# Optimization experiments

Hardware: AMD Instinct MI355X
Metric: run time of the kernel (lower is better)

## Reference

```python
import jax, jax.numpy as jnp
import numpy as np

IN_DIM = 256
OUT_DIM = 256
EMBED_DIM = 256
GROUPS = 8
BN_EPS = 1e-5


def conv2d(x, w, b, pad, groups=1):
    # x: NCHW, w: OIHW (I = in_ch / groups)
    out = jax.lax.conv_general_dilated(
        x, w, window_strides=(1, 1), padding=[(pad, pad), (pad, pad)],
        dimension_numbers=('NCHW', 'OIHW', 'NCHW'), feature_group_count=groups)
    return out + b[None, :, None, None]


def setup_inputs() -> dict:
    key = jax.random.key(0)
    ks = jax.random.split(key, 8)
    s = 0.05
    d = {}
    d['x'] = jax.random.normal(ks[0], (2, IN_DIM, 16, 16), jnp.float32)
    d['y'] = jax.random.normal(ks[1], (2, OUT_DIM, 128, 128), jnp.float32)
    # channle_reduce: Conv2d(256, 64, k=3, groups=64) -> weight (64, 4, 3, 3)
    d['w_cr'] = jax.random.normal(ks[2], (IN_DIM // 4, 4, 3, 3), jnp.float32) * s
    d['b_cr'] = jnp.zeros((IN_DIM // 4,), jnp.float32)
    # depthwise convs on 64 channels
    d['w_dw3'] = jax.random.normal(ks[3], (IN_DIM // 4, 1, 3, 3), jnp.float32) * s
    d['b_dw3'] = jnp.zeros((IN_DIM // 4,), jnp.float32)
    d['w_dw7'] = jax.random.normal(ks[4], (IN_DIM // 4, 1, 5, 5), jnp.float32) * s
    d['b_dw7'] = jnp.zeros((IN_DIM // 4,), jnp.float32)
    # gate: Conv2d(256, 128, 1) + BN + StarReLU
    d['w_gate'] = jax.random.normal(ks[5], (IN_DIM // 2, IN_DIM, 1, 1), jnp.float32) * s
    d['b_gate'] = jnp.zeros((IN_DIM // 2,), jnp.float32)
    d['bn_gamma'] = jnp.ones((IN_DIM // 2,), jnp.float32)
    d['bn_beta'] = jnp.zeros((IN_DIM // 2,), jnp.float32)
    d['bn_mean'] = jnp.zeros((IN_DIM // 2,), jnp.float32)
    d['bn_var'] = jnp.ones((IN_DIM // 2,), jnp.float32)
    d['sr_scale'] = jnp.ones((1,), jnp.float32)
    d['sr_bias'] = jnp.zeros((1,), jnp.float32)
    # linear1: Linear(16, 8192) -> torch weight shape (8192, 16)
    d['w_lin'] = jax.random.normal(ks[6], (OUT_DIM * EMBED_DIM // GROUPS, IN_DIM // (2 * GROUPS)), jnp.float32) * s
    d['b_lin'] = jnp.zeros((OUT_DIM * EMBED_DIM // GROUPS,), jnp.float32)
    return d


def reference(x, y, w_cr, b_cr, w_dw3, b_dw3, w_dw7, b_dw7, w_gate, b_gate,
              bn_gamma, bn_beta, bn_mean, bn_var, sr_scale, sr_bias, w_lin, b_lin):
    B, C, H, Wd = x.shape
    # gate branch: 1x1 conv -> BN (inference stats) -> StarReLU
    g = conv2d(x, w_gate, b_gate, 0)
    inv = (bn_gamma / jnp.sqrt(bn_var + BN_EPS))[None, :, None, None]
    g = (g - bn_mean[None, :, None, None]) * inv + bn_beta[None, :, None, None]
    g = sr_scale * jnp.square(jnp.maximum(g, 0.0)) + sr_bias
    # feature branch
    xr = conv2d(x, w_cr, b_cr, 1, groups=IN_DIM // 4)        # (B, 64, H, W)
    x3 = conv2d(xr, w_dw3, b_dw3, 1, groups=IN_DIM // 4)
    x7 = conv2d(xr, w_dw7, b_dw7, 2, groups=IN_DIM // 4)
    xc = jnp.concatenate([x3, x7], axis=1) * g               # (B, 128, H, W)
    # per-pixel weight generation: (B,H,W,G,16) @ (16,8192)
    xc = xc.reshape(B, GROUPS, -1, H, Wd).transpose(0, 3, 4, 1, 2)
    wdec = jnp.einsum('bhwgi,oi->bhwgo', xc, w_lin) + b_lin  # (B,H,W,8,8192)
    # flatten (G, out*embed/G) -> (embed, out); matches torch reshape order
    wdec = wdec.reshape(B, H, Wd, EMBED_DIM, OUT_DIM)
    # patch-wise dynamic 1x1 conv == per-patch batched matmul
    b, c, h, w = y.shape
    fh, fw = H, Wd
    ph, pw = h // fh, w // fw
    yp = y.reshape(b, c, fh, ph, fw, pw)
    # out[b,e,f,p,g,q] = sum_c wdec[b,f,g,e,c] * y[b,c,f,p,g,q]
    out = jnp.einsum('bfgec,bcfpgq->befpgq', wdec, yp)
    return out.reshape(b, EMBED_DIM, h, w)
```

## Files before the change

### kernel.cpp

```cpp
#include <hip/hip_runtime.h>
#include <stdint.h>


typedef __attribute__((ext_vector_type(8))) short short8;
typedef __attribute__((ext_vector_type(4))) float f32x4;

#define BN_EPS 1e-5f

__device__ __forceinline__ unsigned short f2bf(float f) {
  unsigned u = __float_as_uint(f);
  return (unsigned short)((u + 0x8000u) >> 16);
}
__device__ __forceinline__ unsigned pk2bf(float a, float b) {
  unsigned ua = __float_as_uint(a), ub = __float_as_uint(b);
  return ((ua + 0x8000u) >> 16) | ((ub + 0x8000u) & 0xFFFF0000u);
}

__global__ __launch_bounds__(256) void k1a_groupconv(
    const float* __restrict__ x, const float* __restrict__ w_cr,
    const float* __restrict__ b_cr, float* __restrict__ xr)
{
  __shared__ float xs[4][256];
  int b = blockIdx.x >> 6, cr = blockIdx.x & 63;
  int t = threadIdx.x;
  {
    int ch = t >> 6, off = (t & 63) * 4;
    float4 v = *(const float4*)(x + b * 65536 + (cr * 4 + ch) * 256 + off);
    *(float4*)&xs[ch][off] = v;
  }
  __syncthreads();
  int h = t >> 4, w = t & 15;
  float a = b_cr[cr];
  #pragma unroll
  for (int ii = 0; ii < 4; ++ii) {
    const float* wp = w_cr + (cr * 4 + ii) * 9;
    #pragma unroll
    for (int ky = 0; ky < 3; ++ky) {
      int gy = h + ky - 1;
      #pragma unroll
      for (int kx = 0; kx < 3; ++kx) {
        int gx = w + kx - 1;
        float v = (gy >= 0 && gy < 16 && gx >= 0 && gx < 16) ? xs[ii][gy * 16 + gx] : 0.f;
        a += wp[ky * 3 + kx] * v;
      }
    }
  }
  xr[(b * 64 + cr) * 256 + t] = a;
}

__global__ __launch_bounds__(256) void k1b_gate_dw(
    const float* __restrict__ x, const float* __restrict__ xr,
    const float* __restrict__ w_dw3, const float* __restrict__ b_dw3,
    const float* __restrict__ w_dw7, const float* __restrict__ b_dw7,
    const float* __restrict__ w_gate, const float* __restrict__ b_gate,
    const float* __restrict__ bn_gamma, const float* __restrict__ bn_beta,
    const float* __restrict__ bn_mean, const float* __restrict__ bn_var,
    const float* __restrict__ sr_scale, const float* __restrict__ sr_bias,
    const float* __restrict__ w_lin, short* __restrict__ wlin_bf, short* __restrict__ xc_bf)
{
  __shared__ float xcen[256];
  __shared__ float gs[128];
  int blk = blockIdx.x;
  int b = blk >> 8, h = (blk >> 4) & 15, w = blk & 15;
  int t = threadIdx.x;

  { int idx = blk * 256 + t; wlin_bf[idx] = (short)f2bf(w_lin[idx]); }

  xcen[t] = x[b * 65536 + t * 256 + h * 16 + w];
  __syncthreads();

  int o = t >> 1, half = t & 1;
  {
    const float* wrow = w_gate + o * 256 + half * 128;
    const float* xcn  = xcen + half * 128;
    float ga = 0.f;
    #pragma unroll 8
    for (int ci = 0; ci < 128; ci += 4) {
      float4 wv = *(const float4*)(wrow + ci);
      float4 xv = *(const float4*)(xcn + ci);
      ga += wv.x * xv.x + wv.y * xv.y + wv.z * xv.z + wv.w * xv.w;
    }
    ga += __shfl_xor(ga, 1);
    float inv = bn_gamma[o] * rsqrtf(bn_var[o] + BN_EPS);
    float gg = (ga + b_gate[o] - bn_mean[o]) * inv + bn_beta[o];
    gg = fmaxf(gg, 0.f);
    gg = sr_scale[0] * gg * gg + sr_bias[0];
    if (half == 0) gs[o] = gg;
  }
  __syncthreads();

  if (t < 128) {
    int oc = t;
    float f0;
    if (oc < 64) {
      f0 = b_dw3[oc];
      const float* wp = w_dw3 + oc * 9;
      const float* xp = xr + (b * 64 + oc) * 256;
      #pragma unroll
      for (int ky = 0; ky < 3; ++ky) {
        int gy = h + ky - 1;
        #pragma unroll
        for (int kx = 0; kx < 3; ++kx) {
          int gx = w + kx - 1;
          float v = (gy >= 0 && gy < 16 && gx >= 0 && gx < 16) ? xp[gy * 16 + gx] : 0.f;
          f0 += wp[ky * 3 + kx] * v;
        }
      }
    } else {
      int c5 = oc - 64;
      f0 = b_dw7[c5];
      const float* wp = w_dw7 + c5 * 25;
      const float* xp = xr + (b * 64 + c5) * 256;
      #pragma unroll
      for (int ky = 0; ky < 5; ++ky) {
        int gy = h + ky - 2;
        #pragma unroll
        for (int kx = 0; kx < 5; ++kx) {
          int gx = w + kx - 2;
          float v = (gy >= 0 && gy < 16 && gx >= 0 && gx < 16) ? xp[gy * 16 + gx] : 0.f;
          f0 += wp[ky * 5 + kx] * v;
        }
      }
    }
    int pix = (b * 16 + h) * 16 + w;
    xc_bf[pix * 128 + oc] = (short)f2bf(f0 * gs[oc]);
  }
}

__global__ __launch_bounds__(256) void k2a_wgen(
    const short* __restrict__ wlin_bf, const short* __restrict__ xc_bf,
    const float* __restrict__ b_lin, short* __restrict__ wd)
{
  __shared__ __align__(16) short Wt[16 * 2048];
  int blk = blockIdx.x;
  int n0 = (blk >> 2) * 16;
  int oc = (blk & 3) * 2048;
  int tid = threadIdx.x;
  int wave = tid >> 6, lane = tid & 63;
  int quad = lane >> 4, l16 = lane & 15;

  short8 af = {0, 0, 0, 0, 0, 0, 0, 0};
  if (quad < 2) af = *(const short8*)(xc_bf + (n0 + l16) * 16 + quad * 8);

  f32x4 zero4 = {0.f, 0.f, 0.f, 0.f};
  #pragma unroll 8
  for (int i = 0; i < 32; ++i) {
    int o0 = wave * 512 + i * 16;
    short8 bf = {0, 0, 0, 0, 0, 0, 0, 0};
    if (quad < 2) bf = *(const short8*)(wlin_bf + (oc + o0 + l16) * 16 + quad * 8);
    f32x4 d = __builtin_amdgcn_mfma_f32_16x16x32_bf16(af, bf, zero4, 0, 0, 0);
    float bl = b_lin[oc + o0 + l16];
    #pragma unroll
    for (int r = 0; r < 4; ++r)
      Wt[(quad * 4 + r) * 2048 + o0 + l16] = (short)f2bf(d[r] + bl);
  }
  __syncthreads();

  const uint2* src = (const uint2*)Wt;
  #pragma unroll 8
  for (int j = 0; j < 32; ++j) {
    int fl = j * 256 + tid;
    int row = fl >> 9;
    int col = (fl & 511) * 4;
    *(uint2*)(wd + (size_t)(n0 + row) * 8192 + oc + col) = src[fl];
  }
}

__global__ __launch_bounds__(512, 6) void k2b_dynconv(
    const float* __restrict__ y, const short* __restrict__ wd,
    float* __restrict__ out)
{
  __shared__ __align__(16) short Ylds[16384];
  __shared__ __align__(16) float scratch[4096];

  int phys = blockIdx.x;
  int blk = (phys & 7) * 64 + (phys >> 3);
  int b = blk >> 8, f = (blk >> 4) & 15, g = blk & 15;
  int tid = threadIdx.x;
  int wave = tid >> 6, lane = tid & 63;
  int quad = lane >> 4, l16 = lane & 15;

  const float* yb = y + b * 4194304 + (f * 8) * 128 + g * 8;
  const short* wdp = wd + (size_t)(((b * 16 + f) * 16 + g)) * 65536;

  int c_a = (tid >> 4) & 63;
  (void)c_a;
  float4 v0, v1, w0, w1;
  {
    int task0 = tid, task1 = 512 + tid;
    int ca = task0 >> 4, pfa = task0 & 15;
    int cb = task1 >> 4, pfb = task1 & 15;
    v0 = *(const float4*)(yb + ca * 16384 + (pfa >> 1) * 128 + (pfa & 1) * 4);
    v1 = *(const float4*)(yb + cb * 16384 + (pfb >> 1) * 128 + (pfb & 1) * 4);
  }
  for (int pass = 0; pass < 4; ++pass) {
    {
      int task0 = tid, task1 = 512 + tid;
      int ca = task0 >> 4, pfa = task0 & 15;
      int cb = task1 >> 4, pfb = task1 & 15;
      *(float4*)&scratch[ca * 64 + pfa * 4] = v0;
      *(float4*)&scratch[cb * 64 + pfb * 4] = v1;
      if (pass < 3) {
        w0 = *(const float4*)(yb + ((pass + 1) * 64 + ca) * 16384 + (pfa >> 1) * 128 + (pfa & 1) * 4);
        w1 = *(const float4*)(yb + ((pass + 1) * 64 + cb) * 16384 + (pfb >> 1) * 128 + (pfb & 1) * 4);
      }
    }
    __syncthreads();
    {
      int pix = tid & 63, cg = tid >> 6;
      float s0 = scratch[(cg * 8 + 0) * 64 + pix];
      float s1 = scratch[(cg * 8 + 1) * 64 + pix];
      float s2 = scratch[(cg * 8 + 2) * 64 + pix];
      float s3 = scratch[(cg * 8 + 3) * 64 + pix];
      float s4 = scratch[(cg * 8 + 4) * 64 + pix];
      float s5 = scratch[(cg * 8 + 5) * 64 + pix];
      float s6 = scratch[(cg * 8 + 6) * 64 + pix];
      float s7 = scratch[(cg * 8 + 7) * 64 + pix];
      uint4 pk;
      pk.x = pk2bf(s0, s1); pk.y = pk2bf(s2, s3);
      pk.z = pk2bf(s4, s5); pk.w = pk2bf(s6, s7);
      int chunk = pass * 8 + cg;
      int physc = chunk ^ (pix & 7);
      *(uint4*)&Ylds[pix * 256 + physc * 8] = pk;
    }
    __syncthreads();
    v0 = w0; v1 = w1;
  }

  f32x4 acc[2][4];
  f32x4 zero4 = {0.f, 0.f, 0.f, 0.f};
  #pragma unroll
  for (int et = 0; et < 2; ++et)
    #pragma unroll
    for (int nt = 0; nt < 4; ++nt)
      acc[et][nt] = zero4;

  #pragma unroll 2
  for (int cc = 0; cc < 8; ++cc) {
    short8 A[2], Bf[4];
    #pragma unroll
    for (int et = 0; et < 2; ++et) {
      int e = wave * 32 + et * 16 + l16;
      A[et] = *(const short8*)(wdp + e * 256 + cc * 32 + quad * 8);
    }
    int chunk = cc * 4 + quad;
    #pragma unroll
    for (int nt = 0; nt < 4; ++nt) {
      int nn = nt * 16 + l16;
      int physc = chunk ^ (nn & 7);
      Bf[nt] = *(const short8*)&Ylds[nn * 256 + physc * 8];
    }
    #pragma unroll
    for (int et = 0; et < 2; ++et)
      #pragma unroll
      for (int nt = 0; nt < 4; ++nt)
        acc[et][nt] = __builtin_amdgcn_mfma_f32_16x16x32_bf16(A[et], Bf[nt], acc[et][nt], 0, 0, 0);
  }

  float* ob = out + b * 4194304 + (f * 8) * 128 + g * 8;
  #pragma unroll
  for (int et = 0; et < 2; ++et) {
    int e0 = wave * 32 + et * 16 + quad * 4;
    #pragma unroll
    for (int nt = 0; nt < 4; ++nt) {
      int pix = nt * 16 + l16;
      float* oa = ob + (pix >> 3) * 128 + (pix & 7);
      #pragma unroll
      for (int r = 0; r < 4; ++r)
        oa[(e0 + r) * 16384] = acc[et][nt][r];
    }
  }
}

extern "C" void kernel_launch(void* const* d_in, const int* in_sizes, int n_in,
                              void* d_out, int out_size, void* d_ws, size_t ws_size,
                              hipStream_t stream) {
  const float* x        = (const float*)d_in[0];
  const float* y        = (const float*)d_in[1];
  const float* w_cr     = (const float*)d_in[2];
  const float* b_cr     = (const float*)d_in[3];
  const float* w_dw3    = (const float*)d_in[4];
  const float* b_dw3    = (const float*)d_in[5];
  const float* w_dw7    = (const float*)d_in[6];
  const float* b_dw7    = (const float*)d_in[7];
  const float* w_gate   = (const float*)d_in[8];
  const float* b_gate   = (const float*)d_in[9];
  const float* bn_gamma = (const float*)d_in[10];
  const float* bn_beta  = (const float*)d_in[11];
  const float* bn_mean  = (const float*)d_in[12];
  const float* bn_var   = (const float*)d_in[13];
  const float* sr_scale = (const float*)d_in[14];
  const float* sr_bias  = (const float*)d_in[15];
  const float* w_lin    = (const float*)d_in[16];
  const float* b_lin    = (const float*)d_in[17];
  float* out = (float*)d_out;

  short* xc_bf   = (short*)d_ws;
  short* wlin_bf = (short*)((char*)d_ws + 131072);
  float* xr      = (float*)((char*)d_ws + 131072 + 262144);
  short* wd      = (short*)((char*)d_ws + 131072 + 262144 + 131072);

  hipLaunchKernelGGL(k1a_groupconv, dim3(128), dim3(256), 0, stream, x, w_cr, b_cr, xr);
  hipLaunchKernelGGL(k1b_gate_dw, dim3(512), dim3(256), 0, stream,
                     x, xr, w_dw3, b_dw3, w_dw7, b_dw7, w_gate, b_gate,
                     bn_gamma, bn_beta, bn_mean, bn_var, sr_scale, sr_bias,
                     w_lin, wlin_bf, xc_bf);
  hipLaunchKernelGGL(k2a_wgen, dim3(1024), dim3(256), 0, stream,
                     wlin_bf, xc_bf, b_lin, wd);
  hipLaunchKernelGGL(k2b_dynconv, dim3(512), dim3(512), 0, stream, y, wd, out);
}
```

Measured before the change: 174.5 us.

## Split dynamic-conv blocks into half-patches to double grid size

The dynamic 1x1 conv kernel now launches 1024 blocks, each handling half of an 8x8 patch (4 rows, 32 pixels) instead of the full patch. Shared Y staging is halved, and the software-prefetch double buffering of y loads is removed in favour of two simple load passes. The aim is more parallelism and occupancy across CUs. The cost is that each per-patch weight matrix (wd) is now read by two blocks, which doubles weight traffic, and there is less MFMA work per loaded A fragment.

Result: slower. 180.6 us (+3.5%).

```diff
diff --git a/kernel.cpp b/kernel.cpp
--- a/kernel.cpp
+++ b/kernel.cpp
@@ -170,74 +170,64 @@
     const float* __restrict__ y, const short* __restrict__ wd,
     float* __restrict__ out)
 {
-  __shared__ __align__(16) short Ylds[16384];
+  __shared__ __align__(16) short Ylds[8192];
   __shared__ __align__(16) float scratch[4096];
 
   int phys = blockIdx.x;
-  int blk = (phys & 7) * 64 + (phys >> 3);
-  int b = blk >> 8, f = (blk >> 4) & 15, g = blk & 15;
+  int x_ = phys & 7, q_ = phys >> 3;
+  int sub = q_ & 3, pphi = q_ >> 2;
+  int pp = pphi * 8 + x_;
+  int b = pp >> 7, f = (pp >> 3) & 15, gp = pp & 7;
+  int g = gp * 2 + (sub & 1);
+  int half = sub >> 1;
+
   int tid = threadIdx.x;
   int wave = tid >> 6, lane = tid & 63;
   int quad = lane >> 4, l16 = lane & 15;
 
-  const float* yb = y + b * 4194304 + (f * 8) * 128 + g * 8;
+  const float* yb = y + b * 4194304 + (f * 8 + half * 4) * 128 + g * 8;
   const short* wdp = wd + (size_t)(((b * 16 + f) * 16 + g)) * 65536;
 
-  int c_a = (tid >> 4) & 63;
-  (void)c_a;
-  float4 v0, v1, w0, w1;
-  {
-    int task0 = tid, task1 = 512 + tid;
-    int ca = task0 >> 4, pfa = task0 & 15;
-    int cb = task1 >> 4, pfb = task1 & 15;
-    v0 = *(const float4*)(yb + ca * 16384 + (pfa >> 1) * 128 + (pfa & 1) * 4);
-    v1 = *(const float4*)(yb + cb * 16384 + (pfb >> 1) * 128 + (pfb & 1) * 4);
-  }
-  for (int pass = 0; pass < 4; ++pass) {
-    {
-      int task0 = tid, task1 = 512 + tid;
-      int ca = task0 >> 4, pfa = task0 & 15;
-      int cb = task1 >> 4, pfb = task1 & 15;
-      *(float4*)&scratch[ca * 64 + pfa * 4] = v0;
-      *(float4*)&scratch[cb * 64 + pfb * 4] = v1;
-      if (pass < 3) {
-        w0 = *(const float4*)(yb + ((pass + 1) * 64 + ca) * 16384 + (pfa >> 1) * 128 + (pfa & 1) * 4);
-        w1 = *(const float4*)(yb + ((pass + 1) * 64 + cb) * 16384 + (pfb >> 1) * 128 + (pfb & 1) * 4);
-      }
+  for (int pass = 0; pass < 2; ++pass) {
+    #pragma unroll
+    for (int it = 0; it < 2; ++it) {
+      int task = it * 512 + tid;
+      int c = task >> 3, pf = task & 7;
+      float4 v = *(const float4*)(yb + (pass * 128 + c) * 16384 + (pf >> 1) * 128 + (pf & 3 & 1) * 4);
+      *(float4*)&scratch[c * 32 + pf * 4] = v;
     }
     __syncthreads();
     {
-      int pix = tid & 63, cg = tid >> 6;
-      float s0 = scratch[(cg * 8 + 0) * 64 + pix];
-      float s1 = scratch[(cg * 8 + 1) * 64 + pix];
-      float s2 = scratch[(cg * 8 + 2) * 64 + pix];
-      float s3 = scratch[(cg * 8 + 3) * 64 + pix];
-      float s4 = scratch[(cg * 8 + 4) * 64 + pix];
-      float s5 = scratch[(cg * 8 + 5) * 64 + pix];
-      float s6 = scratch[(cg * 8 + 6) * 64 + pix];
-      float s7 = scratch[(cg * 8 + 7) * 64 + pix];
+      int pix = tid & 31, cg = tid >> 5;
+      float s0 = scratch[(cg * 8 + 0) * 32 + pix];
+      float s1 = scratch[(cg * 8 + 1) * 32 + pix];
+      float s2 = scratch[(cg * 8 + 2) * 32 + pix];
+      float s3 = scratch[(cg * 8 + 3) * 32 + pix];
+      float s4 = scratch[(cg * 8 + 4) * 32 + pix];
+      float s5 = scratch[(cg * 8 + 5) * 32 + pix];
+      float s6 = scratch[(cg * 8 + 6) * 32 + pix];
+      float s7 = scratch[(cg * 8 + 7) * 32 + pix];
       uint4 pk;
       pk.x = pk2bf(s0, s1); pk.y = pk2bf(s2, s3);
       pk.z = pk2bf(s4, s5); pk.w = pk2bf(s6, s7);
-      int chunk = pass * 8 + cg;
+      int chunk = pass * 16 + cg;
       int physc = chunk ^ (pix & 7);
       *(uint4*)&Ylds[pix * 256 + physc * 8] = pk;
     }
     __syncthreads();
-    v0 = w0; v1 = w1;
-  }
-
-  f32x4 acc[2][4];
+  }
+
+  f32x4 acc[2][2];
   f32x4 zero4 = {0.f, 0.f, 0.f, 0.f};
   #pragma unroll
   for (int et = 0; et < 2; ++et)
     #pragma unroll
-    for (int nt = 0; nt < 4; ++nt)
+    for (int nt = 0; nt < 2; ++nt)
       acc[et][nt] = zero4;
 
   #pragma unroll 2
   for (int cc = 0; cc < 8; ++cc) {
-    short8 A[2], Bf[4];
+    short8 A[2], Bf[2];
     #pragma unroll
     for (int et = 0; et < 2; ++et) {
       int e = wave * 32 + et * 16 + l16;
@@ -245,7 +235,7 @@
     }
     int chunk = cc * 4 + quad;
     #pragma unroll
-    for (int nt = 0; nt < 4; ++nt) {
+    for (int nt = 0; nt < 2; ++nt) {
       int nn = nt * 16 + l16;
       int physc = chunk ^ (nn & 7);
       Bf[nt] = *(const short8*)&Ylds[nn * 256 + physc * 8];
@@ -253,16 +243,16 @@
     #pragma unroll
     for (int et = 0; et < 2; ++et)
       #pragma unroll
-      for (int nt = 0; nt < 4; ++nt)
+      for (int nt = 0; nt < 2; ++nt)
         acc[et][nt] = __builtin_amdgcn_mfma_f32_16x16x32_bf16(A[et], Bf[nt], acc[et][nt], 0, 0, 0);
   }
 
-  float* ob = out + b * 4194304 + (f * 8) * 128 + g * 8;
+  float* ob = out + b * 4194304 + (f * 8 + half * 4) * 128 + g * 8;
   #pragma unroll
   for (int et = 0; et < 2; ++et) {
     int e0 = wave * 32 + et * 16 + quad * 4;
     #pragma unroll
-    for (int nt = 0; nt < 4; ++nt) {
+    for (int nt = 0; nt < 2; ++nt) {
       int pix = nt * 16 + l16;
       float* oa = ob + (pix >> 3) * 128 + (pix & 7);
       #pragma unroll
@@ -307,5 +297,5 @@
                      w_lin, wlin_bf, xc_bf);
   hipLaunchKernelGGL(k2a_wgen, dim3(1024), dim3(256), 0, stream,
                      wlin_bf, xc_bf, b_lin, wd);
-  hipLaunchKernelGGL(k2b_dynconv, dim3(512), dim3(512), 0, stream, y, wd, out);
-}
+  hipLaunchKernelGGL(k2b_dynconv, dim3(1024), dim3(512), 0, stream, y, wd, out);
+}
```
